# Performance work log

Hardware: AMD Instinct MI355X
Metric: run time of the kernel (lower is better)

The kernel has to match this reference:

```python
import jax, jax.numpy as jnp
from jax import lax
import numpy as np

H = 50  # hidden_size


def _lstm_layer(x, W_ih, W_hh, b_ih, b_hh):
    """PyTorch-convention LSTM layer. x: [B,T,I]; returns [B,T,H].
    Gate order in the stacked weights is (i, f, g, o), as in torch."""
    B = x.shape[0]
    # Precompute input projections for all timesteps: [B,T,4H]
    xg = jnp.einsum('bti,gi->btg', x, W_ih) + b_ih
    h0 = jnp.zeros((B, H), x.dtype)
    c0 = jnp.zeros((B, H), x.dtype)

    def step(carry, xg_t):
        h, c = carry
        gates = xg_t + h @ W_hh.T + b_hh  # [B,4H]
        i, f, g, o = jnp.split(gates, 4, axis=-1)
        i = jax.nn.sigmoid(i)
        f = jax.nn.sigmoid(f)
        g = jnp.tanh(g)
        o = jax.nn.sigmoid(o)
        c = f * c + i * g
        h = o * jnp.tanh(c)
        return (h, c), h

    (_, _), ys = lax.scan(step, (h0, c0), jnp.swapaxes(xg, 0, 1))  # ys: [T,B,H]
    return jnp.swapaxes(ys, 0, 1)


def setup_inputs() -> dict:
    key = jax.random.key(0)
    ks = jax.random.split(key, 16)
    B, T, I = 4096, 512, 1
    s = 1.0 / np.sqrt(H)
    u = lambda k, shp: jax.random.uniform(k, shp, jnp.float32, -s, s)
    return {
        'x': jax.random.normal(ks[0], (B, T, I), jnp.float32),
        # layer 0 (input_size=1)
        'W_ih0': u(ks[1], (4 * H, I)),
        'W_hh0': u(ks[2], (4 * H, H)),
        'b_ih0': u(ks[3], (4 * H,)),
        'b_hh0': u(ks[4], (4 * H,)),
        # layer 1 (input_size=H)
        'W_ih1': u(ks[5], (4 * H, H)),
        'W_hh1': u(ks[6], (4 * H, H)),
        'b_ih1': u(ks[7], (4 * H,)),
        'b_hh1': u(ks[8], (4 * H,)),
        # MLP head
        'W1': jax.random.normal(ks[9], (32, H), jnp.float32) * 0.1,
        'b1': jnp.zeros((32,), jnp.float32),
        'W2': jax.random.normal(ks[10], (16, 32), jnp.float32) * 0.1,
        'b2': jnp.zeros((16,), jnp.float32),
        'W3': jax.random.normal(ks[11], (1, 16), jnp.float32) * 0.1,
        'b3': jnp.zeros((1,), jnp.float32),
    }


def reference(x, W_ih0, W_hh0, b_ih0, b_hh0, W_ih1, W_hh1, b_ih1, b_hh1,
              W1, b1, W2, b2, W3, b3):
    # 2-layer LSTM (eval mode: inter-layer dropout is identity)
    h = _lstm_layer(x, W_ih0, W_hh0, b_ih0, b_hh0)
    h = _lstm_layer(h, W_ih1, W_hh1, b_ih1, b_hh1)
    out = h[:, -1, :]  # last timestep, [B,H]
    out = jax.nn.relu(out @ W1.T + b1)
    out = jax.nn.relu(out @ W2.T + b2)
    out = out @ W3.T + b3  # [B,1]
    return out
```

## Files before the change

kernel.cpp:

```cpp
#include <hip/hip_runtime.h>

#define TT 512
#define HH 50
#define BT 16
#define AK 136
#define GS 420
#define XC 64
#define XSS 68

typedef __attribute__((ext_vector_type(8))) short bf16x8;
typedef __attribute__((ext_vector_type(4))) float f32x4;

__device__ __forceinline__ float sigf(float x)  { return 1.0f / (1.0f + __expf(-x)); }
__device__ __forceinline__ float tanhfast(float x) { return 1.0f - 2.0f / (__expf(2.0f * x) + 1.0f); }

__device__ __forceinline__ unsigned short bf16hi(float f) {
    unsigned u = __float_as_uint(f);
    return (unsigned short)((u + 0x7fffu + ((u >> 16) & 1u)) >> 16);
}
__device__ __forceinline__ float bf16tof(unsigned short s) {
    return __uint_as_float(((unsigned)s) << 16);
}

__global__ __launch_bounds__(512, 2)
void lstm2_mfma_kernel(const float* __restrict__ x,
                       const float* __restrict__ W_ih0, const float* __restrict__ W_hh0,
                       const float* __restrict__ b_ih0, const float* __restrict__ b_hh0,
                       const float* __restrict__ W_ih1, const float* __restrict__ W_hh1,
                       const float* __restrict__ b_ih1, const float* __restrict__ b_hh1,
                       const float* __restrict__ W1, const float* __restrict__ b1,
                       const float* __restrict__ W2, const float* __restrict__ b2,
                       const float* __restrict__ W3, const float* __restrict__ b3,
                       float* __restrict__ out)
{
    const int tid  = threadIdx.x;
    const int lane = tid & 63;
    const int wid  = tid >> 6;
    const int l15  = lane & 15;
    const int grp8 = (lane >> 4) * 8;
    const int b0   = blockIdx.x * BT;

    __shared__ float          xs[BT][XSS];
    __shared__ unsigned short Ah[BT][AK];
    __shared__ unsigned short Al[BT][AK];
    __shared__ float          gates[BT][GS];
    __shared__ float          h1f[BT][52];
    __shared__ float          bias0s[200], bias1s[200], wih0s[200];
    __shared__ float          D1[BT][32], D2[BT][16];

    if (tid < 200) {
        bias0s[tid] = b_ih0[tid] + b_hh0[tid];
        bias1s[tid] = b_ih1[tid] + b_hh1[tid];
        wih0s[tid]  = W_ih0[tid];
    }
    for (int i = tid; i < BT * AK; i += 512) {
        ((unsigned short*)Ah)[i] = 0;
        ((unsigned short*)Al)[i] = 0;
    }

    int t0, t1, t2, t3;
    if      (wid < 5)  { t0 = 13 + 2 * wid; t1 = 14 + 2 * wid; t2 = wid; t3 = -1; }
    else if (wid == 5) { t0 = 23; t1 = 5;  t2 = 6;  t3 = 7;  }
    else if (wid == 6) { t0 = 24; t1 = 8;  t2 = 9;  t3 = 10; }
    else               { t0 = 25; t1 = 11; t2 = 12; t3 = -1; }
    const int tiles[4] = {t0, t1, t2, t3};

    bf16x8 wHi[4][4], wLo[4][4];
#pragma unroll
    for (int s = 0; s < 4; ++s) {
        const int tl = tiles[s];
        if (tl < 0) continue;
        const int nc   = (tl < 13) ? 2 : 4;
        const int colv = tl * 16 + l15;
#pragma unroll
        for (int c = 0; c < 4; ++c) {
            if (c >= nc) continue;
#pragma unroll
            for (int j = 0; j < 8; ++j) {
                const int kk = 32 * c + grp8 + j;
                float wv = 0.0f;
                if (colv < 200) {
                    if (kk < 50) wv = W_hh0[colv * 50 + kk];
                } else if (colv >= 208 && colv < 408) {
                    const int g1 = colv - 208;
                    if      (kk < 50)  wv = W_ih1[g1 * 50 + kk];
                    else if (kk < 100) wv = W_hh1[g1 * 50 + (kk - 50)];
                }
                const unsigned short h = bf16hi(wv);
                wHi[s][c][j] = (short)h;
                wLo[s][c][j] = (short)bf16hi(wv - bf16tof(h));
            }
        }
    }

    float cst[4] = {0.f, 0.f, 0.f, 0.f};
    __syncthreads();

    for (int tau = 0; tau <= TT; ++tau) {
        if ((tau & (XC - 1)) == 0 && tau < TT && tid < 256) {
            const int r = tid >> 4, q = tid & 15;
            const float4 v = *(const float4*)&x[(size_t)(b0 + r) * TT + tau + 4 * q];
            xs[r][4 * q + 0] = v.x; xs[r][4 * q + 1] = v.y;
            xs[r][4 * q + 2] = v.z; xs[r][4 * q + 3] = v.w;
        }

        bf16x8 ah[4], al[4];
#pragma unroll
        for (int c = 0; c < 4; ++c) {
            ah[c] = *(const bf16x8*)&Ah[l15][32 * c + grp8];
            al[c] = *(const bf16x8*)&Al[l15][32 * c + grp8];
        }
        f32x4 acc[4];
#pragma unroll
        for (int s = 0; s < 4; ++s)
#pragma unroll
            for (int r = 0; r < 4; ++r) acc[s][r] = 0.0f;

#pragma unroll
        for (int s = 0; s < 4; ++s) {
            const int tl = tiles[s];
            if (tl < 0) continue;
            const int nc = (tl < 13) ? 2 : 4;
#pragma unroll
            for (int c = 0; c < 4; ++c) {
                if (c >= nc) continue;
                acc[s] = __builtin_amdgcn_mfma_f32_16x16x32_bf16(ah[c], wHi[s][c], acc[s], 0, 0, 0);
                acc[s] = __builtin_amdgcn_mfma_f32_16x16x32_bf16(al[c], wHi[s][c], acc[s], 0, 0, 0);
                acc[s] = __builtin_amdgcn_mfma_f32_16x16x32_bf16(ah[c], wLo[s][c], acc[s], 0, 0, 0);
            }
        }
#pragma unroll
        for (int s = 0; s < 4; ++s) {
            const int tl = tiles[s];
            if (tl < 0) continue;
            const int col = tl * 16 + l15;
#pragma unroll
            for (int r = 0; r < 4; ++r)
                gates[(lane >> 4) * 4 + r][col] = acc[s][r];
        }
        __syncthreads();

#pragma unroll
        for (int p = 0; p < 4; ++p) {
            const bool on = (p < 3) || (tid < 64);
            if (on) {
                const int q    = (p < 3) ? (tid + (p << 9)) : (1536 + tid);
                const int lay  = (q >= 800) ? 1 : 0;
                const int qq   = lay ? q - 800 : q;
                const int row  = qq & 15;
                const int unit = qq >> 4;
                const bool doit = lay ? (tau >= 1) : (tau < TT);
                if (doit) {
                    const int cb = lay ? 208 : 0;
                    float g0 = gates[row][cb + unit];
                    float g1 = gates[row][cb + 50 + unit];
                    float g2 = gates[row][cb + 100 + unit];
                    float g3 = gates[row][cb + 150 + unit];
                    if (!lay) {
                        const float xv = xs[row][tau & (XC - 1)];
                        g0 = fmaf(xv, wih0s[unit],       g0) + bias0s[unit];
                        g1 = fmaf(xv, wih0s[50 + unit],  g1) + bias0s[50 + unit];
                        g2 = fmaf(xv, wih0s[100 + unit], g2) + bias0s[100 + unit];
                        g3 = fmaf(xv, wih0s[150 + unit], g3) + bias0s[150 + unit];
                    } else {
                        g0 += bias1s[unit];        g1 += bias1s[50 + unit];
                        g2 += bias1s[100 + unit];  g3 += bias1s[150 + unit];
                    }
                    const float ig = sigf(g0), fg = sigf(g1);
                    const float gg = tanhfast(g2), og = sigf(g3);
                    cst[p] = fmaf(fg, cst[p], ig * gg);
                    const float h = og * tanhfast(cst[p]);
                    const unsigned short hh = bf16hi(h);
                    const int kpos = lay ? (50 + unit) : unit;
                    Ah[row][kpos] = hh;
                    Al[row][kpos] = bf16hi(h - bf16tof(hh));
                    if (lay) h1f[row][unit] = h;
                }
            }
        }
        __syncthreads();
    }

    {
        const int r = tid >> 5, o = tid & 31;
        float z = b1[o];
#pragma unroll
        for (int k = 0; k < HH; ++k) z = fmaf(W1[o * HH + k], h1f[r][k], z);
        D1[r][o] = fmaxf(z, 0.0f);
    }
    __syncthreads();
    if (tid < 256) {
        const int r = tid >> 4, o = tid & 15;
        float z = b2[o];
#pragma unroll
        for (int k = 0; k < 32; ++k) z = fmaf(W2[o * 32 + k], D1[r][k], z);
        D2[r][o] = fmaxf(z, 0.0f);
    }
    __syncthreads();
    if (tid < BT) {
        float z = b3[0];
#pragma unroll
        for (int k = 0; k < 16; ++k) z = fmaf(W3[k], D2[tid][k], z);
        out[b0 + tid] = z;
    }
}

extern "C" void kernel_launch(void* const* d_in, const int* in_sizes, int n_in,
                              void* d_out, int out_size, void* d_ws, size_t ws_size,
                              hipStream_t stream) {
    const float* x     = (const float*)d_in[0];
    const float* W_ih0 = (const float*)d_in[1];
    const float* W_hh0 = (const float*)d_in[2];
    const float* b_ih0 = (const float*)d_in[3];
    const float* b_hh0 = (const float*)d_in[4];
    const float* W_ih1 = (const float*)d_in[5];
    const float* W_hh1 = (const float*)d_in[6];
    const float* b_ih1 = (const float*)d_in[7];
    const float* b_hh1 = (const float*)d_in[8];
    const float* W1    = (const float*)d_in[9];
    const float* b1    = (const float*)d_in[10];
    const float* W2    = (const float*)d_in[11];
    const float* b2    = (const float*)d_in[12];
    const float* W3    = (const float*)d_in[13];
    const float* b3    = (const float*)d_in[14];

    const int B = in_sizes[0] / TT;
    const int nblocks = B / BT;

    lstm2_mfma_kernel<<<dim3(nblocks), dim3(512), 0, stream>>>(
        x, W_ih0, W_hh0, b_ih0, b_hh0, W_ih1, W_hh1, b_ih1, b_hh1,
        W1, b1, W2, b2, W3, b3, (float*)d_out);
}
```

Measured before the change: 1.211 ms.

## Swap MFMA operands so gates land in registers; fold input and bias into GEMM

Weights become the A operand, with rows permuted so each lane's accumulator holds the i,f,g,o gates for one unit. The cell update can then run directly in registers, which drops the shared gates buffer and one of the two barriers per timestep. The layer-0 input projection and both biases are folded into the MFMA by adding x and a constant-one column to the hidden-state buffer. That buffer is now double-buffered, and x for the next step is prefetched by a single quarter-wave. The trade-off is more MFMA work, since padded units and wave assignments are less balanced, and each x load goes to global memory every step.

```diff
diff --git a/kernel.cpp b/kernel.cpp
--- a/kernel.cpp
+++ b/kernel.cpp
@@ -4,14 +4,13 @@
 #define HH 50
 #define BT 16
 #define AK 136
-#define GS 420
-#define XC 64
-#define XSS 68
 
 typedef __attribute__((ext_vector_type(8))) short bf16x8;
+typedef __attribute__((ext_vector_type(4))) short s16x4;
+typedef __attribute__((ext_vector_type(2))) short s16x2;
 typedef __attribute__((ext_vector_type(4))) float f32x4;
 
-__device__ __forceinline__ float sigf(float x)  { return 1.0f / (1.0f + __expf(-x)); }
+__device__ __forceinline__ float sigf(float x)     { return 1.0f / (1.0f + __expf(-x)); }
 __device__ __forceinline__ float tanhfast(float x) { return 1.0f - 2.0f / (__expf(2.0f * x) + 1.0f); }
 
 __device__ __forceinline__ unsigned short bf16hi(float f) {
@@ -23,68 +22,61 @@
 }
 
 __global__ __launch_bounds__(512, 2)
-void lstm2_mfma_kernel(const float* __restrict__ x,
-                       const float* __restrict__ W_ih0, const float* __restrict__ W_hh0,
-                       const float* __restrict__ b_ih0, const float* __restrict__ b_hh0,
-                       const float* __restrict__ W_ih1, const float* __restrict__ W_hh1,
-                       const float* __restrict__ b_ih1, const float* __restrict__ b_hh1,
-                       const float* __restrict__ W1, const float* __restrict__ b1,
-                       const float* __restrict__ W2, const float* __restrict__ b2,
-                       const float* __restrict__ W3, const float* __restrict__ b3,
-                       float* __restrict__ out)
+void lstm2_mfma2_kernel(const float* __restrict__ x,
+                        const float* __restrict__ W_ih0, const float* __restrict__ W_hh0,
+                        const float* __restrict__ b_ih0, const float* __restrict__ b_hh0,
+                        const float* __restrict__ W_ih1, const float* __restrict__ W_hh1,
+                        const float* __restrict__ b_ih1, const float* __restrict__ b_hh1,
+                        const float* __restrict__ W1, const float* __restrict__ b1,
+                        const float* __restrict__ W2, const float* __restrict__ b2,
+                        const float* __restrict__ W3, const float* __restrict__ b3,
+                        float* __restrict__ out)
 {
-    const int tid  = threadIdx.x;
-    const int lane = tid & 63;
-    const int wid  = tid >> 6;
-    const int l15  = lane & 15;
-    const int grp8 = (lane >> 4) * 8;
-    const int b0   = blockIdx.x * BT;
-
-    __shared__ float          xs[BT][XSS];
-    __shared__ unsigned short Ah[BT][AK];
-    __shared__ unsigned short Al[BT][AK];
-    __shared__ float          gates[BT][GS];
-    __shared__ float          h1f[BT][52];
-    __shared__ float          bias0s[200], bias1s[200], wih0s[200];
-    __shared__ float          D1[BT][32], D2[BT][16];
-
-    if (tid < 200) {
-        bias0s[tid] = b_ih0[tid] + b_hh0[tid];
-        bias1s[tid] = b_ih1[tid] + b_hh1[tid];
-        wih0s[tid]  = W_ih0[tid];
-    }
-    for (int i = tid; i < BT * AK; i += 512) {
-        ((unsigned short*)Ah)[i] = 0;
-        ((unsigned short*)Al)[i] = 0;
-    }
-
-    int t0, t1, t2, t3;
-    if      (wid < 5)  { t0 = 13 + 2 * wid; t1 = 14 + 2 * wid; t2 = wid; t3 = -1; }
-    else if (wid == 5) { t0 = 23; t1 = 5;  t2 = 6;  t3 = 7;  }
-    else if (wid == 6) { t0 = 24; t1 = 8;  t2 = 9;  t3 = 10; }
-    else               { t0 = 25; t1 = 11; t2 = 12; t3 = -1; }
-    const int tiles[4] = {t0, t1, t2, t3};
-
+    const int tid   = threadIdx.x;
+    const int lane  = tid & 63;
+    const int wid   = tid >> 6;
+    const int gp    = lane >> 4;
+    const int l15   = lane & 15;
+    const int grp8  = gp * 8;
+    const int layer = wid >> 2;
+    const int ubase = (wid & 3) * 16;
+    const int b0    = blockIdx.x * BT;
+
+    __shared__ unsigned short Ah[2][BT][AK];
+    __shared__ unsigned short Al[2][BT][AK];
+    __shared__ float h1f[BT][52];
+    __shared__ float D1[BT][32], D2[BT][16];
+
+    {
+        unsigned* az = (unsigned*)Ah;
+        unsigned* bz = (unsigned*)Al;
+        for (int i = tid; i < 2 * BT * (AK / 2); i += 512) { az[i] = 0u; bz[i] = 0u; }
+    }
+
+    const int gateA = l15 & 3;
+    const int unitA = ubase + (l15 >> 2) * 4;
     bf16x8 wHi[4][4], wLo[4][4];
 #pragma unroll
     for (int s = 0; s < 4; ++s) {
-        const int tl = tiles[s];
-        if (tl < 0) continue;
-        const int nc   = (tl < 13) ? 2 : 4;
-        const int colv = tl * 16 + l15;
 #pragma unroll
         for (int c = 0; c < 4; ++c) {
-            if (c >= nc) continue;
+            if (layer == 0 && c >= 2) continue;
+            const int u  = unitA + s;
+            const int gu = gateA * HH + u;
 #pragma unroll
             for (int j = 0; j < 8; ++j) {
                 const int kk = 32 * c + grp8 + j;
                 float wv = 0.0f;
-                if (colv < 200) {
-                    if (kk < 50) wv = W_hh0[colv * 50 + kk];
-                } else if (colv >= 208 && colv < 408) {
-                    const int g1 = colv - 208;
-                    if      (kk < 50)  wv = W_ih1[g1 * 50 + kk];
-                    else if (kk < 100) wv = W_hh1[g1 * 50 + (kk - 50)];
+                if (u < HH) {
+                    if (layer == 0) {
+                        if      (kk < 50)  wv = W_hh0[gu * HH + kk];
+                        else if (kk == 50) wv = W_ih0[gu];
+                        else if (kk == 51) wv = b_ih0[gu] + b_hh0[gu];
+                    } else {
+                        if      (kk < 50)  wv = W_ih1[gu * HH + kk];
+                        else if (kk == 51) wv = b_ih1[gu] + b_hh1[gu];
+                        else if (kk >= 52 && kk < 102) wv = W_hh1[gu * HH + (kk - 52)];
+                    }
                 }
                 const unsigned short h = bf16hi(wv);
                 wHi[s][c][j] = (short)h;
@@ -93,90 +85,91 @@
         }
     }
 
+    __syncthreads();
+    if (tid < 32) Ah[tid >> 4][tid & 15][51] = 0x3F80;
+    if (tid < BT) {
+        const float xv = x[(size_t)(b0 + tid) * TT];
+        const unsigned short xh = bf16hi(xv);
+        Ah[0][tid][50] = xh;
+        Al[0][tid][50] = bf16hi(xv - bf16tof(xh));
+    }
+    __syncthreads();
+
     float cst[4] = {0.f, 0.f, 0.f, 0.f};
-    __syncthreads();
+    const int u0 = ubase + 4 * gp;
+    const int nv = (u0 + 3 < HH) ? 4 : ((u0 < HH) ? 2 : 0);
 
     for (int tau = 0; tau <= TT; ++tau) {
-        if ((tau & (XC - 1)) == 0 && tau < TT && tid < 256) {
-            const int r = tid >> 4, q = tid & 15;
-            const float4 v = *(const float4*)&x[(size_t)(b0 + r) * TT + tau + 4 * q];
-            xs[r][4 * q + 0] = v.x; xs[r][4 * q + 1] = v.y;
-            xs[r][4 * q + 2] = v.z; xs[r][4 * q + 3] = v.w;
+        const int cur = tau & 1, nxt = cur ^ 1;
+        const bool active = layer ? (tau >= 1) : (tau < TT);
+        const bool xduty  = (wid == 3 && gp == 1 && tau < TT - 1);
+
+        float xv = 0.0f;
+        if (xduty) xv = x[(size_t)(b0 + l15) * TT + (tau + 1)];
+
+        if (active) {
+            bf16x8 bh0, bh1, bh2, bh3, bl0, bl1, bl2, bl3;
+            bh0 = *(const bf16x8*)&Ah[cur][l15][grp8];
+            bh1 = *(const bf16x8*)&Ah[cur][l15][32 + grp8];
+            bl0 = *(const bf16x8*)&Al[cur][l15][grp8];
+            bl1 = *(const bf16x8*)&Al[cur][l15][32 + grp8];
+            if (layer) {
+                bh2 = *(const bf16x8*)&Ah[cur][l15][64 + grp8];
+                bh3 = *(const bf16x8*)&Ah[cur][l15][96 + grp8];
+                bl2 = *(const bf16x8*)&Al[cur][l15][64 + grp8];
+                bl3 = *(const bf16x8*)&Al[cur][l15][96 + grp8];
+            }
+
+            f32x4 acc[4];
+#pragma unroll
+            for (int s = 0; s < 4; ++s) { acc[s][0] = acc[s][1] = acc[s][2] = acc[s][3] = 0.f; }
+
+#define EFT(S, C, BH, BL)                                                              \
+    acc[S] = __builtin_amdgcn_mfma_f32_16x16x32_bf16(wHi[S][C], BH, acc[S], 0, 0, 0);  \
+    acc[S] = __builtin_amdgcn_mfma_f32_16x16x32_bf16(wHi[S][C], BL, acc[S], 0, 0, 0);  \
+    acc[S] = __builtin_amdgcn_mfma_f32_16x16x32_bf16(wLo[S][C], BH, acc[S], 0, 0, 0);
+
+            EFT(0,0,bh0,bl0) EFT(1,0,bh0,bl0) EFT(2,0,bh0,bl0) EFT(3,0,bh0,bl0)
+            EFT(0,1,bh1,bl1) EFT(1,1,bh1,bl1) EFT(2,1,bh1,bl1) EFT(3,1,bh1,bl1)
+            if (layer) {
+                EFT(0,2,bh2,bl2) EFT(1,2,bh2,bl2) EFT(2,2,bh2,bl2) EFT(3,2,bh2,bl2)
+                EFT(0,3,bh3,bl3) EFT(1,3,bh3,bl3) EFT(2,3,bh3,bl3) EFT(3,3,bh3,bl3)
+            }
+#undef EFT
+
+            unsigned short hh[4], hl[4];
+            float hf[4];
+#pragma unroll
+            for (int s = 0; s < 4; ++s) {
+                const float ig = sigf(acc[s][0]);
+                const float fg = sigf(acc[s][1]);
+                const float gg = tanhfast(acc[s][2]);
+                const float og = sigf(acc[s][3]);
+                cst[s] = fmaf(fg, cst[s], ig * gg);
+                const float h = og * tanhfast(cst[s]);
+                hf[s] = h;
+                hh[s] = bf16hi(h);
+                hl[s] = bf16hi(h - bf16tof(hh[s]));
+            }
+
+            const int kpos = (layer ? 52 : 0) + u0;
+            if (nv == 4) {
+                *(s16x4*)&Ah[nxt][l15][kpos] = (s16x4){(short)hh[0], (short)hh[1], (short)hh[2], (short)hh[3]};
+                *(s16x4*)&Al[nxt][l15][kpos] = (s16x4){(short)hl[0], (short)hl[1], (short)hl[2], (short)hl[3]};
+            } else if (nv == 2) {
+                *(s16x2*)&Ah[nxt][l15][kpos] = (s16x2){(short)hh[0], (short)hh[1]};
+                *(s16x2*)&Al[nxt][l15][kpos] = (s16x2){(short)hl[0], (short)hl[1]};
+            }
+            if (layer && tau == TT && nv) {
+                if (nv == 4) *(float4*)&h1f[l15][u0] = make_float4(hf[0], hf[1], hf[2], hf[3]);
+                else         { h1f[l15][u0] = hf[0]; h1f[l15][u0 + 1] = hf[1]; }
+            }
         }
 
-        bf16x8 ah[4], al[4];
-#pragma unroll
-        for (int c = 0; c < 4; ++c) {
-            ah[c] = *(const bf16x8*)&Ah[l15][32 * c + grp8];
-            al[c] = *(const bf16x8*)&Al[l15][32 * c + grp8];
-        }
-        f32x4 acc[4];
-#pragma unroll
-        for (int s = 0; s < 4; ++s)
-#pragma unroll
-            for (int r = 0; r < 4; ++r) acc[s][r] = 0.0f;
-
-#pragma unroll
-        for (int s = 0; s < 4; ++s) {
-            const int tl = tiles[s];
-            if (tl < 0) continue;
-            const int nc = (tl < 13) ? 2 : 4;
-#pragma unroll
-            for (int c = 0; c < 4; ++c) {
-                if (c >= nc) continue;
-                acc[s] = __builtin_amdgcn_mfma_f32_16x16x32_bf16(ah[c], wHi[s][c], acc[s], 0, 0, 0);
-                acc[s] = __builtin_amdgcn_mfma_f32_16x16x32_bf16(al[c], wHi[s][c], acc[s], 0, 0, 0);
-                acc[s] = __builtin_amdgcn_mfma_f32_16x16x32_bf16(ah[c], wLo[s][c], acc[s], 0, 0, 0);
-            }
-        }
-#pragma unroll
-        for (int s = 0; s < 4; ++s) {
-            const int tl = tiles[s];
-            if (tl < 0) continue;
-            const int col = tl * 16 + l15;
-#pragma unroll
-            for (int r = 0; r < 4; ++r)
-                gates[(lane >> 4) * 4 + r][col] = acc[s][r];
-        }
-        __syncthreads();
-
-#pragma unroll
-        for (int p = 0; p < 4; ++p) {
-            const bool on = (p < 3) || (tid < 64);
-            if (on) {
-                const int q    = (p < 3) ? (tid + (p << 9)) : (1536 + tid);
-                const int lay  = (q >= 800) ? 1 : 0;
-                const int qq   = lay ? q - 800 : q;
-                const int row  = qq & 15;
-                const int unit = qq >> 4;
-                const bool doit = lay ? (tau >= 1) : (tau < TT);
-                if (doit) {
-                    const int cb = lay ? 208 : 0;
-                    float g0 = gates[row][cb + unit];
-                    float g1 = gates[row][cb + 50 + unit];
-                    float g2 = gates[row][cb + 100 + unit];
-                    float g3 = gates[row][cb + 150 + unit];
-                    if (!lay) {
-                        const float xv = xs[row][tau & (XC - 1)];
-                        g0 = fmaf(xv, wih0s[unit],       g0) + bias0s[unit];
-                        g1 = fmaf(xv, wih0s[50 + unit],  g1) + bias0s[50 + unit];
-                        g2 = fmaf(xv, wih0s[100 + unit], g2) + bias0s[100 + unit];
-                        g3 = fmaf(xv, wih0s[150 + unit], g3) + bias0s[150 + unit];
-                    } else {
-                        g0 += bias1s[unit];        g1 += bias1s[50 + unit];
-                        g2 += bias1s[100 + unit];  g3 += bias1s[150 + unit];
-                    }
-                    const float ig = sigf(g0), fg = sigf(g1);
-                    const float gg = tanhfast(g2), og = sigf(g3);
-                    cst[p] = fmaf(fg, cst[p], ig * gg);
-                    const float h = og * tanhfast(cst[p]);
-                    const unsigned short hh = bf16hi(h);
-                    const int kpos = lay ? (50 + unit) : unit;
-                    Ah[row][kpos] = hh;
-                    Al[row][kpos] = bf16hi(h - bf16tof(hh));
-                    if (lay) h1f[row][unit] = h;
-                }
-            }
+        if (xduty) {
+            const unsigned short xh = bf16hi(xv);
+            Ah[nxt][l15][50] = xh;
+            Al[nxt][l15][50] = bf16hi(xv - bf16tof(xh));
         }
         __syncthreads();
     }
@@ -227,7 +220,7 @@
     const int B = in_sizes[0] / TT;
     const int nblocks = B / BT;
 
-    lstm2_mfma_kernel<<<dim3(nblocks), dim3(512), 0, stream>>>(
+    lstm2_mfma2_kernel<<<dim3(nblocks), dim3(512), 0, stream>>>(
         x, W_ih0, W_hh0, b_ih0, b_hh0, W_ih1, W_hh1, b_ih1, b_hh1,
         W1, b1, W2, b2, W3, b3, (float*)d_out);
 }
```

After: 1.057 ms. 1.15x faster.
